# Kernel tuning notes

Measured on AMD Instinct MI355X. Metric: run time of the kernel, lower is better.

Reference implementation:

```python
import jax, jax.numpy as jnp
import numpy as np

CIN, COUT, K = 64, 64, 3
ALPHA = 8.3
STRIDE, PAD, DIL = 1, 1, 1
B, H = 8, 128


def _unfold(x, k, dilation, padding, stride):
    # torch.nn.functional.unfold: output feature order is (C, kh, kw)
    x = jnp.pad(x, ((0, 0), (0, 0), (padding, padding), (padding, padding)))
    b, c, h, w = x.shape
    eff = dilation * (k - 1) + 1
    oh = (h - eff) // stride + 1
    ow = (w - eff) // stride + 1
    cols = []
    for i in range(k):
        for j in range(k):
            cols.append(x[:, :, i * dilation:i * dilation + stride * oh:stride,
                              j * dilation:j * dilation + stride * ow:stride])
    p = jnp.stack(cols, axis=2)          # [B, C, k*k, oh, ow]
    return p.reshape(b, c * k * k, oh * ow)


def setup_inputs() -> dict:
    key = jax.random.key(0)
    k1, k2, k3, k4 = jax.random.split(key, 4)
    image = jax.random.normal(k1, (B, CIN, H, H), dtype=jnp.float32)
    depth = jax.random.uniform(k2, (B, 1, H, H), dtype=jnp.float32)
    weight = jax.random.normal(k3, (COUT, CIN, K, K), dtype=jnp.float32) * 0.05
    bias = jax.random.normal(k4, (COUT,), dtype=jnp.float32) * 0.05
    return {"image": image, "depth": depth, "weight": weight, "bias": bias}


def reference(image, depth, weight, bias):
    # im2col of the image: [B, L, Cin*k*k]
    patches = _unfold(image, K, DIL, PAD, STRIDE).transpose(0, 2, 1)
    b, L, _ = patches.shape
    # depth is repeat()'d to Cin channels in the original; the unfolded depth
    # columns therefore tile the single-channel patch Cin times. Exploit that:
    dpatch = _unfold(depth, K, DIL, PAD, STRIDE).transpose(0, 2, 1)  # [B, L, k*k]
    # original centre index: int((Cin*k*k)/2); within the tiled patch this is
    # position (Cin*k*k//2) % (k*k) of the single-channel patch
    centre_idx = (CIN * K * K // 2) % (K * K)
    centre = dpatch[:, :, centre_idx:centre_idx + 1]
    sim = jnp.exp(-ALPHA * jnp.abs(dpatch - centre))  # [B, L, k*k]
    # modulate per kernel offset (broadcast over channels == tiled similarity)
    modulated = patches.reshape(b, L, CIN, K * K) * sim[:, :, None, :]
    out = jnp.einsum('blck,ock->blo', modulated, weight.reshape(COUT, CIN, K * K))
    out = out + bias
    osz = (image.shape[-1] + 2 * PAD - DIL * (K - 1) - 1) // STRIDE + 1
    return out.transpose(0, 2, 1).reshape(b, COUT, osz, osz)
```

## Files before the change

kernel.cpp:

```cpp
#include <hip/hip_runtime.h>
#include <hip/hip_bf16.h>

#define BATCH 8
#define CIN   64
#define COUT  64
#define HH    128
#define WW    128
#define HW    (HH * WW)
#define ALPHA 8.3f
#define TPX   64
#define XW    66

typedef __attribute__((ext_vector_type(8))) short short8;
typedef __attribute__((ext_vector_type(4))) float f32x4;

__device__ __forceinline__ int img_idx(int r, int x, int c) {
    return (((r * XW + x) << 6) + c) ^ ((x & 7) << 3);
}

__global__ __launch_bounds__(256)
void transpose_w(const float* __restrict__ w, __hip_bfloat16* __restrict__ wt) {
    int i = blockIdx.x * 256 + threadIdx.x;
    if (i >= 9 * 64 * 64) return;
    int c = i & 63;
    int o = (i >> 6) & 63;
    int tap = i >> 12;
    wt[i] = __float2bfloat16(w[(o * 64 + c) * 9 + tap]);
}

__global__ __launch_bounds__(512)
void depthconv_fused(const float* __restrict__ image,
                     const float* __restrict__ depth,
                     const float* __restrict__ bias,
                     const short* __restrict__ wt,
                     float* __restrict__ out) {
    __shared__ short s_img[6 * XW * 64];
    __shared__ float s_d[6][XW];
    __shared__ float s_sim[4][9][TPX];

    const int tid = threadIdx.x;
    const int bid = ((blockIdx.x & 7) << 6) | (blockIdx.x >> 3);
    const int yg = bid & 31;
    const int xt = (bid >> 5) & 1;
    const int b  = bid >> 6;
    const int x0 = xt * TPX;
    const int y0 = yg * 4;

    const int lane = tid & 63;
    const int wid  = tid >> 6;
    const int l15  = lane & 15;
    const int lq   = lane >> 4;
    const int og   = wid & 3;
    const int pr   = wid >> 2;
    const int o_base = og * 16;

    if (wid < 6) {
        const int sx  = 1 + lane;
        const int gy  = y0 - 1 + wid;
        const bool yok = (unsigned)gy < HH;
        const int gx  = x0 + lane;
        const float* ip = &image[((b * CIN) * HH + (yok ? gy : 0)) * WW + gx];
        const int base = (wid * XW + sx) << 6;
        const int swz  = (sx & 7) << 3;
        #pragma unroll 16
        for (int c2 = 0; c2 < 32; ++c2) {
            float v0 = ip[0], v1 = ip[HW];
            if (!yok) { v0 = 0.f; v1 = 0.f; }
            ip += 2 * HW;
            __hip_bfloat162 pk = __float22bfloat162_rn(float2{v0, v1});
            *(__hip_bfloat162*)&s_img[base + ((2 * c2) ^ swz)] = pk;
        }
    } else if (wid == 6) {
        if (lane < 12) {
            const int rr = lane >> 1, e = lane & 1;
            const int sx = e ? (XW - 1) : 0;
            const int gy = y0 - 1 + rr;
            const int gx = x0 - 1 + sx;
            const bool ok = (unsigned)gy < HH && (unsigned)gx < WW;
            const float* p = &image[((b * CIN) * HH + (ok ? gy : 0)) * WW + (ok ? gx : 0)];
            #pragma unroll 8
            for (int c2 = 0; c2 < 32; ++c2) {
                float v0 = p[0], v1 = p[HW];
                if (!ok) { v0 = 0.f; v1 = 0.f; }
                p += 2 * HW;
                __hip_bfloat162 pk = __float22bfloat162_rn(float2{v0, v1});
                *(__hip_bfloat162*)&s_img[img_idx(rr, sx, 2 * c2)] = pk;
            }
        }
    } else {
        for (int i = lane; i < 6 * XW; i += 64) {
            int rr = i / XW, x = i - rr * XW;
            int gy = y0 - 1 + rr, gx = x0 - 1 + x;
            float v = 0.f;
            if ((unsigned)gy < HH && (unsigned)gx < WW)
                v = depth[(b * HH + gy) * WW + gx];
            s_d[rr][x] = v;
        }
    }
    __syncthreads();

    for (int i = tid; i < 4 * 9 * TPX; i += 512) {
        int p  = i & 63;
        int t  = i >> 6;
        int yy = t / 9, tap = t - yy * 9;
        int ri = tap / 3, dj = tap - ri * 3;
        float dt = s_d[yy + ri][p + dj];
        float dc = s_d[yy][p];
        s_sim[yy][tap][p] = __expf(-ALPHA * fabsf(dt - dc));
    }

    float bias_v[4];
    #pragma unroll
    for (int r = 0; r < 4; ++r) bias_v[r] = bias[o_base + lq * 4 + r];

    __syncthreads();

    f32x4 a0[4], a1[4];
    #pragma unroll
    for (int nt = 0; nt < 4; ++nt) {
        a0[nt] = f32x4{0.f, 0.f, 0.f, 0.f};
        a1[nt] = f32x4{0.f, 0.f, 0.f, 0.f};
    }

    #pragma unroll 1
    for (int r = 0; r < 4; ++r) {
        const int rr = 2 * pr + r;
        #pragma unroll 1
        for (int dj = 0; dj < 3; ++dj) {
            const int t0 = 3 * r + dj;
            const int t1 = 3 * (r - 1) + dj;
            short8 wA00, wA01, wA10, wA11;
            if (r < 3) {
                wA00 = *(const short8*)&wt[(t0 * 64 + o_base + l15) * 64 + lq * 8];
                wA01 = *(const short8*)&wt[(t0 * 64 + o_base + l15) * 64 + 32 + lq * 8];
            }
            if (r >= 1) {
                wA10 = *(const short8*)&wt[(t1 * 64 + o_base + l15) * 64 + lq * 8];
                wA11 = *(const short8*)&wt[(t1 * 64 + o_base + l15) * 64 + 32 + lq * 8];
            }
            #pragma unroll
            for (int nt = 0; nt < 4; ++nt) {
                const int xb = nt * 16 + l15;
                short8 b0 = *(const short8*)&s_img[img_idx(rr, xb + dj, lq * 8)];
                short8 b1 = *(const short8*)&s_img[img_idx(rr, xb + dj, 32 + lq * 8)];
                if (r < 3) {
                    f32x4 t = __builtin_amdgcn_mfma_f32_16x16x32_bf16(
                        wA00, b0, (f32x4){0.f, 0.f, 0.f, 0.f}, 0, 0, 0);
                    t = __builtin_amdgcn_mfma_f32_16x16x32_bf16(wA01, b1, t, 0, 0, 0);
                    const float sv = s_sim[2 * pr][t0][xb];
                    #pragma unroll
                    for (int e = 0; e < 4; ++e) a0[nt][e] = fmaf(sv, t[e], a0[nt][e]);
                }
                if (r >= 1) {
                    f32x4 t = __builtin_amdgcn_mfma_f32_16x16x32_bf16(
                        wA10, b0, (f32x4){0.f, 0.f, 0.f, 0.f}, 0, 0, 0);
                    t = __builtin_amdgcn_mfma_f32_16x16x32_bf16(wA11, b1, t, 0, 0, 0);
                    const float sv = s_sim[2 * pr + 1][t1][xb];
                    #pragma unroll
                    for (int e = 0; e < 4; ++e) a1[nt][e] = fmaf(sv, t[e], a1[nt][e]);
                }
            }
        }
    }

    const int yb = y0 + 2 * pr;
    #pragma unroll
    for (int nt = 0; nt < 4; ++nt) {
        const int px = x0 + nt * 16 + l15;
        #pragma unroll
        for (int rr = 0; rr < 4; ++rr) {
            const int o = o_base + lq * 4 + rr;
            out[((b * COUT + o) * HH + yb) * WW + px]     = a0[nt][rr] + bias_v[rr];
            out[((b * COUT + o) * HH + yb + 1) * WW + px] = a1[nt][rr] + bias_v[rr];
        }
    }
}

extern "C" void kernel_launch(void* const* d_in, const int* in_sizes, int n_in,
                              void* d_out, int out_size, void* d_ws, size_t ws_size,
                              hipStream_t stream) {
    const float* image  = (const float*)d_in[0];
    const float* depth  = (const float*)d_in[1];
    const float* weight = (const float*)d_in[2];
    const float* bias   = (const float*)d_in[3];
    float* out = (float*)d_out;
    __hip_bfloat16* wt = (__hip_bfloat16*)d_ws;

    transpose_w<<<(9 * 64 * 64 + 255) / 256, 256, 0, stream>>>(weight, wt);

    dim3 grid(BATCH * 2 * 32);
    depthconv_fused<<<grid, 512, 0, stream>>>(image, depth, bias,
                                              (const short*)wt, out);
}
```

Before: 108.6 us.

## Spread image tile staging across all warps with float4 loads and add waves_per_eu hint

Replaces the per-warp staging scheme, where six warps each loaded one row with scalar loads over 32 channel-pair iterations, with a layout in which all 512 threads load float4 vectors of two channels across six rows. The halo columns and depth loads are redistributed over thread ranges. The goal is to cut the serialized global load latency in the prologue and make better use of memory bandwidth. It also adds an amdgpu_waves_per_eu(4) attribute, which may constrain register allocation and risks spilling in the MFMA loop.

```diff
diff --git a/kernel.cpp b/kernel.cpp
--- a/kernel.cpp
+++ b/kernel.cpp
@@ -28,7 +28,7 @@
     wt[i] = __float2bfloat16(w[(o * 64 + c) * 9 + tap]);
 }
 
-__global__ __launch_bounds__(512)
+__global__ __launch_bounds__(512) __attribute__((amdgpu_waves_per_eu(4)))
 void depthconv_fused(const float* __restrict__ image,
                      const float* __restrict__ depth,
                      const float* __restrict__ bias,
@@ -54,41 +54,46 @@
     const int pr   = wid >> 2;
     const int o_base = og * 16;
 
-    if (wid < 6) {
-        const int sx  = 1 + lane;
-        const int gy  = y0 - 1 + wid;
-        const bool yok = (unsigned)gy < HH;
-        const int gx  = x0 + lane;
-        const float* ip = &image[((b * CIN) * HH + (yok ? gy : 0)) * WW + gx];
-        const int base = (wid * XW + sx) << 6;
-        const int swz  = (sx & 7) << 3;
-        #pragma unroll 16
-        for (int c2 = 0; c2 < 32; ++c2) {
-            float v0 = ip[0], v1 = ip[HW];
-            if (!yok) { v0 = 0.f; v1 = 0.f; }
-            ip += 2 * HW;
-            __hip_bfloat162 pk = __float22bfloat162_rn(float2{v0, v1});
-            *(__hip_bfloat162*)&s_img[base + ((2 * c2) ^ swz)] = pk;
-        }
-    } else if (wid == 6) {
-        if (lane < 12) {
-            const int rr = lane >> 1, e = lane & 1;
-            const int sx = e ? (XW - 1) : 0;
-            const int gy = y0 - 1 + rr;
-            const int gx = x0 - 1 + sx;
-            const bool ok = (unsigned)gy < HH && (unsigned)gx < WW;
-            const float* p = &image[((b * CIN) * HH + (ok ? gy : 0)) * WW + (ok ? gx : 0)];
-            #pragma unroll 8
-            for (int c2 = 0; c2 < 32; ++c2) {
-                float v0 = p[0], v1 = p[HW];
-                if (!ok) { v0 = 0.f; v1 = 0.f; }
-                p += 2 * HW;
-                __hip_bfloat162 pk = __float22bfloat162_rn(float2{v0, v1});
-                *(__hip_bfloat162*)&s_img[img_idx(rr, sx, 2 * c2)] = pk;
+    {
+        const int x4 = tid & 15;
+        const int c2 = (tid >> 4) & 31;
+        const float* ip0 = &image[((size_t)(b * CIN + 2 * c2) * HH) * WW + x0 + 4 * x4];
+        #pragma unroll
+        for (int r = 0; r < 6; ++r) {
+            const int gy = y0 - 1 + r;
+            const bool yok = (unsigned)gy < HH;
+            const float* p = ip0 + (yok ? gy : 0) * WW;
+            float4 f0 = *(const float4*)p;
+            float4 f1 = *(const float4*)(p + HW);
+            if (!yok) { f0 = float4{0,0,0,0}; f1 = float4{0,0,0,0}; }
+            __hip_bfloat162 pk[4];
+            pk[0] = __float22bfloat162_rn(float2{f0.x, f1.x});
+            pk[1] = __float22bfloat162_rn(float2{f0.y, f1.y});
+            pk[2] = __float22bfloat162_rn(float2{f0.z, f1.z});
+            pk[3] = __float22bfloat162_rn(float2{f0.w, f1.w});
+            #pragma unroll
+            for (int jj = 0; jj < 4; ++jj) {
+                const int j  = (x4 + jj) & 3;
+                const int sx = 1 + 4 * x4 + j;
+                *(__hip_bfloat162*)&s_img[img_idx(r, sx, 2 * c2)] = pk[j];
             }
         }
+    }
+    if (tid < 384) {
+        const int c2 = tid / 12;
+        const int rem = tid - c2 * 12;
+        const int r = rem >> 1, e = rem & 1;
+        const int sx = e ? (XW - 1) : 0;
+        const int gy = y0 - 1 + r;
+        const int gx = x0 - 1 + sx;
+        const bool ok = (unsigned)gy < HH && (unsigned)gx < WW;
+        const float* p = &image[((size_t)(b * CIN + 2 * c2) * HH + (ok ? gy : 0)) * WW + (ok ? gx : 0)];
+        float v0 = p[0], v1 = p[HW];
+        if (!ok) { v0 = 0.f; v1 = 0.f; }
+        *(__hip_bfloat162*)&s_img[img_idx(r, sx, 2 * c2)] =
+            __float22bfloat162_rn(float2{v0, v1});
     } else {
-        for (int i = lane; i < 6 * XW; i += 64) {
+        for (int i = tid - 384; i < 6 * XW; i += 128) {
             int rr = i / XW, x = i - rr * XW;
             int gy = y0 - 1 + rr, gx = x0 - 1 + x;
             float v = 0.f;
```

New measurement: 130.6 us. +20.2%, slower.
